# Kernel tuning notes

Measured on AMD Instinct MI355X. Metric: run time of the kernel, lower is better.

The kernel has to match this reference:

```python
import jax, jax.numpy as jnp
import numpy as np

RADIUS = 0.2
NSAMPLE = 32
BANDWIDTH = 0.1


def ellipsoid_query(xyz, new_xyz, radius, nsample):
    """xyz:(B,N,3), new_xyz:(B,P,3) -> idx:(B,P,nsample) int32.
    Ellipsoid semi-axes (radius, 2*radius, radius); first nsample hits,
    padded with the first hit (index 0 if empty), matching the CUDA kernel.
    """
    B, N, _ = xyz.shape
    inv_sq = jnp.asarray([1.0 / radius**2, 1.0 / (2.0 * radius) ** 2, 1.0 / radius**2],
                         dtype=xyz.dtype)
    # accumulate per-coordinate to avoid a (B,P,N,3) intermediate
    q = jnp.zeros((B, new_xyz.shape[1], N), dtype=xyz.dtype)
    for k in range(3):
        d = new_xyz[:, :, None, k] - xyz[:, None, :, k]  # (B,P,N)
        q = q + d * d * inv_sq[k]
    mask = q < 1.0
    cand = jnp.where(mask, jnp.arange(N, dtype=jnp.int32), jnp.int32(N))  # invalid -> N
    cand = jnp.sort(cand, axis=-1)[..., :nsample]                          # (B,P,S)
    first = cand[..., :1]
    first = jnp.where(first >= N, jnp.int32(0), first)
    return jnp.where(cand >= N, first, cand)


def group(features, idx):
    """features:(B,C,N), idx:(B,P,S) -> (B,C,P,S)"""
    return jnp.take_along_axis(features[:, :, None, :], idx[:, None, :, :], axis=-1)


def setup_inputs() -> dict:
    key = jax.random.key(0)
    k1, k2, k3 = jax.random.split(key, 3)
    xyz = jax.random.uniform(k1, (4, 8192, 3), dtype=jnp.float32)
    new_xyz = jax.random.uniform(k2, (4, 2048, 3), dtype=jnp.float32)
    features = jax.random.normal(k3, (4, 64, 8192), dtype=jnp.float32)
    return {"xyz": xyz, "new_xyz": new_xyz, "features": features}


def reference(xyz, new_xyz, features):
    idx = ellipsoid_query(xyz, new_xyz, RADIUS, NSAMPLE)          # (B,P,S)
    xyz_trans = jnp.transpose(xyz, (0, 2, 1))                      # (B,3,N)
    grouped_xyz = group(xyz_trans, idx)                            # (B,3,P,S)
    # density: gaussian of distance to center
    g = jnp.transpose(grouped_xyz, (0, 2, 3, 1))                   # (B,P,S,3)
    dist = jnp.linalg.norm(g - new_xyz[:, :, None, :], axis=-1)    # (B,P,S)
    density = jnp.exp(-dist**2 / (2.0 * BANDWIDTH**2)) / (2.5 * BANDWIDTH)
    grouped_density = (1.0 / density)[:, None, :, :]               # (B,1,P,S)
    grouped_features = group(features, idx)                        # (B,C,P,S)
    return jnp.concatenate([grouped_xyz, grouped_density, grouped_features], axis=1)
```

## Files before the change

### kernel.cpp

```cpp
#include <hip/hip_runtime.h>

constexpr int NPTS = 8192;
constexpr int NQ   = 2048;
constexpr int NC   = 64;
constexpr int NS   = 32;
constexpr int NCH  = 3 + 1 + NC;
constexpr int CS   = NQ * NS;



union KLds {
    float tile[NC][65];
    int   idx[4][NS];
};

__device__ __forceinline__ unsigned prefix_popc(unsigned long long m) {
    return __builtin_amdgcn_mbcnt_hi((unsigned)(m >> 32),
           __builtin_amdgcn_mbcnt_lo((unsigned)m, 0u));
}

__global__ __launch_bounds__(256, 8) void scan_trans_kernel(
    const float* __restrict__ xyz,
    const float* __restrict__ nxyz,
    const float* __restrict__ feat,
    float* __restrict__ ftr,
    int* __restrict__ gidx,
    float* __restrict__ out,
    int ntrans)
{
    __shared__ KLds u;
    const int bx = blockIdx.x;
    const int t  = threadIdx.x;

    if (bx < ntrans) {
        const int b  = bx >> 7;
        const int tl = bx & 127;
        const int n0 = tl * 64;
        const float* fb = feat + (size_t)b * NC * NPTS;
        {
            const int pl = t & 63;
            const int c0 = t >> 6;
            #pragma unroll
            for (int i = 0; i < 16; ++i) {
                const int c = c0 + 4 * i;
                u.tile[c][pl] = fb[(size_t)c * NPTS + n0 + pl];
            }
        }
        __syncthreads();
        float* tb = ftr + ((size_t)b * NPTS + n0) * NC;
        {
            const int cl = t & 63;
            const int pb = t >> 6;
            #pragma unroll
            for (int i = 0; i < 16; ++i) {
                const int pp = pb + 4 * i;
                tb[(size_t)pp * NC + cl] = u.tile[cl][pp];
            }
        }
        return;
    }

    const int sb   = bx - ntrans;
    const int qpb  = NQ / 4;
    const int b    = sb / qpb;
    const int p0   = (sb - b * qpb) * 4;
    const int lane = t & 63;
    const int wave = t >> 6;
    const int p    = p0 + wave;
    const float* xb = xyz + (size_t)b * NPTS * 3;
    int* idx_row = u.idx[wave];

    const float qx = nxyz[((size_t)b * NQ + p) * 3 + 0];
    const float qy = nxyz[((size_t)b * NQ + p) * 3 + 1];
    const float qz = nxyz[((size_t)b * NQ + p) * 3 + 2];

    int cnt = 0;
    int first = -1;

    float x0 = xb[3 * lane + 0], y0 = xb[3 * lane + 1], z0 = xb[3 * lane + 2];
    float x1 = xb[3 * (64 + lane) + 0], y1 = xb[3 * (64 + lane) + 1],
          z1 = xb[3 * (64 + lane) + 2];

    for (int base = 0; base < NPTS; base += 64) {
        float xn = 0.f, yn = 0.f, zn = 0.f;
        const int pf = base + 128;
        if (pf < NPTS) {
            xn = xb[3 * (pf + lane) + 0];
            yn = xb[3 * (pf + lane) + 1];
            zn = xb[3 * (pf + lane) + 2];
        }

        const float dx = __fsub_rn(qx, x0);
        const float dy = __fsub_rn(qy, y0);
        const float dz = __fsub_rn(qz, z0);
        const float t0 = __fmul_rn(__fmul_rn(dx, dx), 25.0f);
        const float t1 = __fmul_rn(__fmul_rn(dy, dy), 6.25f);
        const float t2 = __fmul_rn(__fmul_rn(dz, dz), 25.0f);
        const float qv = __fadd_rn(__fadd_rn(t0, t1), t2);
        const bool hit = qv < 1.0f;

        const unsigned long long m = __ballot(hit);
        if (first < 0 && m != 0ull)
            first = base + __builtin_ctzll(m);
        if (hit) {
            const int pos = cnt + (int)prefix_popc(m);
            if (pos < NS) idx_row[pos] = base + lane;
        }
        cnt += __popcll(m);
        if (cnt >= NS) break;

        x0 = x1; y0 = y1; z0 = z1;
        x1 = xn; y1 = yn; z1 = zn;
    }
    if (cnt < NS) {
        const int f = (cnt == 0) ? 0 : first;
        if (lane < NS && lane >= cnt) idx_row[lane] = f;
    }

    if (lane < NS) {
        const int s = lane;
        const int j = idx_row[s];
        gidx[((size_t)b * NQ + p) * NS + s] = j;

        const float px = xb[3 * j + 0];
        const float py = xb[3 * j + 1];
        const float pz = xb[3 * j + 2];
        const float dx = __fsub_rn(px, qx);
        const float dy = __fsub_rn(py, qy);
        const float dz = __fsub_rn(pz, qz);
        const float d2 = __fadd_rn(__fadd_rn(__fmul_rn(dx, dx), __fmul_rn(dy, dy)),
                                   __fmul_rn(dz, dz));
        const float dist = __fsqrt_rn(d2);
        const float arg  = __fdiv_rn(-__fmul_rn(dist, dist), 0.02f);
        const float density = __fmul_rn(expf(arg), 4.0f);
        const float gd = __fdiv_rn(1.0f, density);

        float* ob = out + ((size_t)b * NCH * NQ + p) * NS + s;
        ob[0 * (size_t)CS] = px;
        ob[1 * (size_t)CS] = py;
        ob[2 * (size_t)CS] = pz;
        ob[3 * (size_t)CS] = gd;
    }
}

__global__ __launch_bounds__(512, 8) void group_kernel(
    const int* __restrict__ gidx,
    const float* __restrict__ ftr,
    float* __restrict__ out,
    int B)
{
    __shared__ float ldsc[NC][33];

    const int g = blockIdx.x;
    int b, p;
    if (B == 4) {
        b = (g & 7) >> 1;
        p = ((g >> 3) << 1) | (g & 1);
    } else {
        b = g / NQ;
        p = g - b * NQ;
    }
    const int tid = threadIdx.x;

    const int cg = tid & 15;
    const int sl = tid >> 4;
    const int j  = gidx[((size_t)b * NQ + p) * NS + sl];
    const float4 v = ((const float4*)(ftr + ((size_t)b * NPTS + j) * NC))[cg];
    ldsc[4 * cg + 0][sl] = v.x;
    ldsc[4 * cg + 1][sl] = v.y;
    ldsc[4 * cg + 2][sl] = v.z;
    ldsc[4 * cg + 3][sl] = v.w;
    __syncthreads();

    const int c  = tid >> 3;
    const int s4 = (tid & 7) << 2;
    float4 w;
    w.x = ldsc[c][s4 + 0];
    w.y = ldsc[c][s4 + 1];
    w.z = ldsc[c][s4 + 2];
    w.w = ldsc[c][s4 + 3];
    float* op = out + (((size_t)b * NCH + 4 + c) * NQ + p) * NS + s4;
    *(float4*)op = w;
}

__global__ __launch_bounds__(512, 8) void ellip_direct_kernel(
    const float* __restrict__ xyz,
    const float* __restrict__ nxyz,
    const float* __restrict__ feat,
    float* __restrict__ out)
{
    __shared__ int idx_s[8][NS];

    const int b    = blockIdx.y;
    const int p0   = blockIdx.x * 8;
    const int tid  = threadIdx.x;
    const int lane = tid & 63;
    const int wave = tid >> 6;
    const float* xb = xyz + (size_t)b * NPTS * 3;

    {
        const int p = p0 + wave;
        const float qx = nxyz[((size_t)b * NQ + p) * 3 + 0];
        const float qy = nxyz[((size_t)b * NQ + p) * 3 + 1];
        const float qz = nxyz[((size_t)b * NQ + p) * 3 + 2];
        int cnt = 0, first = -1;
        for (int base = 0; base < NPTS; base += 64) {
            const int i = base + lane;
            const float dx = __fsub_rn(qx, xb[i * 3 + 0]);
            const float dy = __fsub_rn(qy, xb[i * 3 + 1]);
            const float dz = __fsub_rn(qz, xb[i * 3 + 2]);
            const float t0 = __fmul_rn(__fmul_rn(dx, dx), 25.0f);
            const float t1 = __fmul_rn(__fmul_rn(dy, dy), 6.25f);
            const float t2 = __fmul_rn(__fmul_rn(dz, dz), 25.0f);
            const float qv = __fadd_rn(__fadd_rn(t0, t1), t2);
            const bool hit = qv < 1.0f;
            const unsigned long long m = __ballot(hit);
            if (first < 0 && m != 0ull) first = base + __builtin_ctzll(m);
            if (hit) {
                const int pos = cnt + __popcll(m & ((1ull << lane) - 1ull));
                if (pos < NS) idx_s[wave][pos] = i;
            }
            cnt += __popcll(m);
            if (cnt >= NS) break;
        }
        if (cnt < NS) {
            const int f = (cnt == 0) ? 0 : first;
            if (lane < NS && lane >= cnt) idx_s[wave][lane] = f;
        }
    }
    __syncthreads();

    const int s = tid & 31;
    const int h = (tid >> 5) & 1;
    const int q = tid >> 6;
    const int p = p0 + q;
    const int j = idx_s[q][s];
    float* ob = out + ((size_t)b * NCH * NQ + p) * NS + s;

    if (h == 0) {
        const float qx = nxyz[((size_t)b * NQ + p) * 3 + 0];
        const float qy = nxyz[((size_t)b * NQ + p) * 3 + 1];
        const float qz = nxyz[((size_t)b * NQ + p) * 3 + 2];
        const float px = xb[j * 3 + 0], py = xb[j * 3 + 1], pz = xb[j * 3 + 2];
        const float dx = __fsub_rn(px, qx);
        const float dy = __fsub_rn(py, qy);
        const float dz = __fsub_rn(pz, qz);
        const float d2 = __fadd_rn(__fadd_rn(__fmul_rn(dx, dx), __fmul_rn(dy, dy)),
                                   __fmul_rn(dz, dz));
        const float dist = __fsqrt_rn(d2);
        const float arg  = __fdiv_rn(-__fmul_rn(dist, dist), 0.02f);
        const float gd = __fdiv_rn(1.0f, __fmul_rn(expf(arg), 4.0f));
        ob[0 * (size_t)CS] = px;
        ob[1 * (size_t)CS] = py;
        ob[2 * (size_t)CS] = pz;
        ob[3 * (size_t)CS] = gd;
    }
    const float* fb = feat + (size_t)b * NC * NPTS + j;
    #pragma unroll 4
    for (int c = h; c < NC; c += 2)
        ob[(size_t)(4 + c) * CS] = fb[(size_t)c * NPTS];
}

extern "C" void kernel_launch(void* const* d_in, const int* in_sizes, int n_in,
                              void* d_out, int out_size, void* d_ws, size_t ws_size,
                              hipStream_t stream) {
    const float* xyz  = (const float*)d_in[0];
    const float* nxyz = (const float*)d_in[1];
    const float* feat = (const float*)d_in[2];
    float* out = (float*)d_out;

    const int B = in_sizes[0] / (NPTS * 3);
    const size_t ftr_f = (size_t)B * NPTS * NC;
    const size_t idx_f = (size_t)B * NQ * NS;
    const size_t need  = (ftr_f + idx_f) * 4;

    if (ws_size >= need) {
        float* ftr = (float*)d_ws;
        int*   idx = (int*)(ftr + ftr_f);

        const int ntrans = B * (NPTS / 64);
        const int nscan  = B * (NQ / 4);
        scan_trans_kernel<<<dim3(ntrans + nscan), 256, 0, stream>>>(
            xyz, nxyz, feat, ftr, idx, out, ntrans);
        group_kernel<<<dim3(B * NQ), 512, 0, stream>>>(idx, ftr, out, B);
    } else {
        ellip_direct_kernel<<<dim3(NQ / 8, B), 512, 0, stream>>>(xyz, nxyz, feat, out);
    }
}
```

Measured before the change: 112.6 us.

## Stage point tiles in LDS shared by eight query waves per block

The ball-query scan now runs eight queries per 512-thread block. Each tile of 2048 points is loaded cooperatively into LDS in SoA layout, so all waves reuse the tile instead of each wave streaming xyz from global memory on its own. The inner loop handles two 64-point chunks per iteration. A shared done-counter lets the block stop early once every wave has its 32 hits. The trade-offs are about 25KB of LDS per block, which lowers occupancy, extra block-wide syncs, and waves that finish early idling until the whole block is done. The transpose blocks are reshaped to match the 512-thread launch.

Measured after the change: 100.2 us. 1.12x faster.

```diff
diff --git a/kernel.cpp b/kernel.cpp
--- a/kernel.cpp
+++ b/kernel.cpp
@@ -6,12 +6,18 @@
 constexpr int NS   = 32;
 constexpr int NCH  = 3 + 1 + NC;
 constexpr int CS   = NQ * NS;
+constexpr int TP   = 2048;
+constexpr int QPB  = 8;
 
 
 
 union KLds {
+    struct {
+        float pts[3][TP + 1];
+        int   idx[QPB][NS];
+        int   ndone;
+    } s;
     float tile[NC][65];
-    int   idx[4][NS];
 };
 
 __device__ __forceinline__ unsigned prefix_popc(unsigned long long m) {
@@ -19,7 +25,7 @@
            __builtin_amdgcn_mbcnt_lo((unsigned)m, 0u));
 }
 
-__global__ __launch_bounds__(256, 8) void scan_trans_kernel(
+__global__ __launch_bounds__(512, 8) void scan_trans_kernel(
     const float* __restrict__ xyz,
     const float* __restrict__ nxyz,
     const float* __restrict__ feat,
@@ -37,38 +43,32 @@
         const int tl = bx & 127;
         const int n0 = tl * 64;
         const float* fb = feat + (size_t)b * NC * NPTS;
-        {
-            const int pl = t & 63;
-            const int c0 = t >> 6;
-            #pragma unroll
-            for (int i = 0; i < 16; ++i) {
-                const int c = c0 + 4 * i;
-                u.tile[c][pl] = fb[(size_t)c * NPTS + n0 + pl];
-            }
+        const int pl = t & 63;
+        const int c0 = t >> 6;
+        #pragma unroll
+        for (int i = 0; i < 8; ++i) {
+            const int c = c0 + 8 * i;
+            u.tile[c][pl] = fb[(size_t)c * NPTS + n0 + pl];
         }
         __syncthreads();
         float* tb = ftr + ((size_t)b * NPTS + n0) * NC;
-        {
-            const int cl = t & 63;
-            const int pb = t >> 6;
-            #pragma unroll
-            for (int i = 0; i < 16; ++i) {
-                const int pp = pb + 4 * i;
-                tb[(size_t)pp * NC + cl] = u.tile[cl][pp];
-            }
+        #pragma unroll
+        for (int i = 0; i < 8; ++i) {
+            const int pp = c0 + 8 * i;
+            tb[(size_t)pp * NC + pl] = u.tile[pl][pp];
         }
         return;
     }
 
     const int sb   = bx - ntrans;
-    const int qpb  = NQ / 4;
+    const int qpb  = NQ / QPB;
     const int b    = sb / qpb;
-    const int p0   = (sb - b * qpb) * 4;
+    const int p0   = (sb - b * qpb) * QPB;
     const int lane = t & 63;
     const int wave = t >> 6;
     const int p    = p0 + wave;
     const float* xb = xyz + (size_t)b * NPTS * 3;
-    int* idx_row = u.idx[wave];
+    int* idx_row = u.s.idx[wave];
 
     const float qx = nxyz[((size_t)b * NQ + p) * 3 + 0];
     const float qy = nxyz[((size_t)b * NQ + p) * 3 + 1];
@@ -76,42 +76,71 @@
 
     int cnt = 0;
     int first = -1;
-
-    float x0 = xb[3 * lane + 0], y0 = xb[3 * lane + 1], z0 = xb[3 * lane + 2];
-    float x1 = xb[3 * (64 + lane) + 0], y1 = xb[3 * (64 + lane) + 1],
-          z1 = xb[3 * (64 + lane) + 2];
-
-    for (int base = 0; base < NPTS; base += 64) {
-        float xn = 0.f, yn = 0.f, zn = 0.f;
-        const int pf = base + 128;
-        if (pf < NPTS) {
-            xn = xb[3 * (pf + lane) + 0];
-            yn = xb[3 * (pf + lane) + 1];
-            zn = xb[3 * (pf + lane) + 2];
-        }
-
-        const float dx = __fsub_rn(qx, x0);
-        const float dy = __fsub_rn(qy, y0);
-        const float dz = __fsub_rn(qz, z0);
-        const float t0 = __fmul_rn(__fmul_rn(dx, dx), 25.0f);
-        const float t1 = __fmul_rn(__fmul_rn(dy, dy), 6.25f);
-        const float t2 = __fmul_rn(__fmul_rn(dz, dz), 25.0f);
-        const float qv = __fadd_rn(__fadd_rn(t0, t1), t2);
-        const bool hit = qv < 1.0f;
-
-        const unsigned long long m = __ballot(hit);
-        if (first < 0 && m != 0ull)
-            first = base + __builtin_ctzll(m);
-        if (hit) {
-            const int pos = cnt + (int)prefix_popc(m);
-            if (pos < NS) idx_row[pos] = base + lane;
-        }
-        cnt += __popcll(m);
-        if (cnt >= NS) break;
-
-        x0 = x1; y0 = y1; z0 = z1;
-        x1 = xn; y1 = yn; z1 = zn;
-    }
+    if (t == 0) u.s.ndone = 0;
+
+    for (int tb = 0; tb < NPTS / TP; ++tb) {
+        const float* src = xb + (size_t)tb * TP * 3;
+        #pragma unroll
+        for (int k = 0; k < 3 * TP / 512; ++k) {
+            const int g  = k * 512 + t;
+            const float val = src[g];
+            const int pt = g / 3;
+            const int c  = g - 3 * pt;
+            u.s.pts[c][pt] = val;
+        }
+        __syncthreads();
+
+        if (cnt < NS) {
+            const int boff = tb * TP;
+            for (int base = 0; base < TP; base += 128) {
+                const int i0 = base + lane;
+                const int i1 = i0 + 64;
+                const float xA = u.s.pts[0][i0], xB = u.s.pts[0][i1];
+                const float yA = u.s.pts[1][i0], yB = u.s.pts[1][i1];
+                const float zA = u.s.pts[2][i0], zB = u.s.pts[2][i1];
+
+                const float dxA = __fsub_rn(qx, xA);
+                const float dyA = __fsub_rn(qy, yA);
+                const float dzA = __fsub_rn(qz, zA);
+                const float qA  = __fadd_rn(__fadd_rn(
+                                    __fmul_rn(__fmul_rn(dxA, dxA), 25.0f),
+                                    __fmul_rn(__fmul_rn(dyA, dyA), 6.25f)),
+                                    __fmul_rn(__fmul_rn(dzA, dzA), 25.0f));
+                const float dxB = __fsub_rn(qx, xB);
+                const float dyB = __fsub_rn(qy, yB);
+                const float dzB = __fsub_rn(qz, zB);
+                const float qB  = __fadd_rn(__fadd_rn(
+                                    __fmul_rn(__fmul_rn(dxB, dxB), 25.0f),
+                                    __fmul_rn(__fmul_rn(dyB, dyB), 6.25f)),
+                                    __fmul_rn(__fmul_rn(dzB, dzB), 25.0f));
+                const bool hitA = qA < 1.0f;
+                const bool hitB = qB < 1.0f;
+
+                const unsigned long long m0 = __ballot(hitA);
+                const unsigned long long m1 = __ballot(hitB);
+                if (first < 0) {
+                    if (m0 != 0ull)      first = boff + base + __builtin_ctzll(m0);
+                    else if (m1 != 0ull) first = boff + base + 64 + __builtin_ctzll(m1);
+                }
+                if (hitA) {
+                    const int pos = cnt + (int)prefix_popc(m0);
+                    if (pos < NS) idx_row[pos] = boff + i0;
+                }
+                const int c0h = __popcll(m0);
+                if (hitB) {
+                    const int pos = cnt + c0h + (int)prefix_popc(m1);
+                    if (pos < NS) idx_row[pos] = boff + i1;
+                }
+                cnt += c0h + __popcll(m1);
+                if (cnt >= NS) break;
+            }
+            if (cnt >= NS && lane == 0)
+                atomicAdd(&u.s.ndone, 1);
+        }
+        __syncthreads();
+        if (u.s.ndone == QPB) break;
+    }
+
     if (cnt < NS) {
         const int f = (cnt == 0) ? 0 : first;
         if (lane < NS && lane >= cnt) idx_row[lane] = f;
@@ -279,8 +308,8 @@
         int*   idx = (int*)(ftr + ftr_f);
 
         const int ntrans = B * (NPTS / 64);
-        const int nscan  = B * (NQ / 4);
-        scan_trans_kernel<<<dim3(ntrans + nscan), 256, 0, stream>>>(
+        const int nscan  = B * (NQ / QPB);
+        scan_trans_kernel<<<dim3(ntrans + nscan), 512, 0, stream>>>(
             xyz, nxyz, feat, ftr, idx, out, ntrans);
         group_kernel<<<dim3(B * NQ), 512, 0, stream>>>(idx, ftr, out, B);
     } else {
```
